# Kernel tuning notes

Hardware: AMD Instinct MI355X
Metric: run time of the kernel (lower is better)

## Reference

```python
import jax, jax.numpy as jnp
import numpy as np

# Note: the original applies F.dropout(p=0.2) after the shared Linear. Dropout is
# omitted here (identity) so the reference is deterministic; this is the eval-mode math.

def setup_inputs() -> dict:
    key = jax.random.key(0)
    k1, k2, k3 = jax.random.split(key, 3)
    B, L, D = 8, 2048, 1024  # D = dim*4 with dim=256
    ix = jax.random.normal(k1, (B, L, D), dtype=jnp.float32)
    iother = jax.random.normal(k2, (B, L, D), dtype=jnp.float32)
    # Linear(dim*4, dim*4) weight/bias, torch convention W: [out, in]
    W = jax.random.normal(k3, (D, D), dtype=jnp.float32) * (1.0 / np.sqrt(D))
    b = jnp.zeros((D,), dtype=jnp.float32)
    return {"ix": ix, "iother": iother, "W": W, "b": b}


def reference(ix, iother, W, b):
    # shared projection (torch Linear: x @ W.T + b)
    ex = ix @ W.T + b            # [B, Lx, D]
    eother = iother @ W.T + b    # [B, Lo, D]
    # cross-attention scores (no scaling, per original)
    align = jnp.einsum('bld,bmd->blm', ex, eother)   # [B, Lx, Lo]
    align = jax.nn.softmax(align, axis=-1)
    # note: values are the RAW iother, not the projected eother
    aligned = jnp.einsum('blm,bmd->bld', align, iother)  # [B, Lx, D]
    return aligned
```

## Files before the change

### kernel.cpp

```cpp
#include <hip/hip_runtime.h>
#include <stdint.h>
#include <stddef.h>


typedef short bf16x8 __attribute__((ext_vector_type(8)));
typedef float f32x4  __attribute__((ext_vector_type(4)));

typedef const __attribute__((address_space(1))) uint32_t* gas_ptr;
typedef __attribute__((address_space(3))) uint32_t* las_ptr;

__device__ __forceinline__ void gl_lds16(const void* g, void* l) {
    __builtin_amdgcn_global_load_lds((gas_ptr)g, (las_ptr)l, 16, 0, 0);
}

__device__ __forceinline__ unsigned short f2bf(float f) {
    union { float f; uint32_t u; } v; v.f = f;
    uint32_t r = v.u + 0x7fffu + ((v.u >> 16) & 1u);
    return (unsigned short)(r >> 16);
}
__device__ __forceinline__ float bf2f(unsigned short h) {
    union { uint32_t u; float f; } v; v.u = ((uint32_t)h) << 16; return v.f;
}

#define L_ 2048
#define D_ 1024
#define ROWB 4096
#define NKT 32
#define SLOT 49152
#define LDSB 32768
#define DYN_LDS (3 * SLOT)
#define SLOT2 65536
#define LDSB2 32768
#define DYN_LDS2 (2 * SLOT2)

__device__ __forceinline__ void xcd_remap(int gx, int gy, int& m, int& n, int& z) {
    const int bid = blockIdx.x + gx * (blockIdx.y + gy * blockIdx.z);
    const int T = gx * gy * (int)gridDim.z;
    const int chunk = T >> 3;
    const int b2 = (bid & 7) * chunk + (bid >> 3);
    m = b2 % gx;
    const int r = b2 / gx;
    n = r % gy;
    z = r / gy;
}

__global__ __launch_bounds__(256) void k_split(
        const float* __restrict__ in, unsigned short* __restrict__ hl, int n4) {
    const int i = blockIdx.x * 256 + threadIdx.x;
    if (i >= n4) return;
    float4 v = ((const float4*)in)[i];
    unsigned short h0 = f2bf(v.x), h1 = f2bf(v.y), h2 = f2bf(v.z), h3 = f2bf(v.w);
    unsigned short l0 = f2bf(v.x - bf2f(h0)), l1 = f2bf(v.y - bf2f(h1));
    unsigned short l2 = f2bf(v.z - bf2f(h2)), l3 = f2bf(v.w - bf2f(h3));
    uint2 hu, lu;
    hu.x = (uint32_t)h0 | ((uint32_t)h1 << 16);
    hu.y = (uint32_t)h2 | ((uint32_t)h3 << 16);
    lu.x = (uint32_t)l0 | ((uint32_t)l1 << 16);
    lu.y = (uint32_t)l2 | ((uint32_t)l3 << 16);
    const int row = i >> 8;
    const int c4 = (i & 255) << 2;
    const size_t o = (size_t)row * 2048 + ((c4 >> 5) << 6) + (c4 & 31);
    *(uint2*)&hl[o]      = hu;
    *(uint2*)&hl[o + 32] = lu;
}

__global__ __launch_bounds__(256) void k_transpose(
        const float* __restrict__ V, unsigned short* __restrict__ Vt) {
    __shared__ unsigned short tile[64][72];
    const int b = blockIdx.z, k0 = blockIdx.x * 64, n0 = blockIdx.y * 64;
    const int t = threadIdx.x;
    const int row = t >> 2, cs = (t & 3) * 16;
    const float* src = V + ((size_t)b * L_ + k0 + row) * D_ + n0 + cs;
#pragma unroll
    for (int q = 0; q < 4; q++) {
        float4 f = ((const float4*)src)[q];
        tile[row][cs + q * 4 + 0] = f2bf(f.x);
        tile[row][cs + q * 4 + 1] = f2bf(f.y);
        tile[row][cs + q * 4 + 2] = f2bf(f.z);
        tile[row][cs + q * 4 + 3] = f2bf(f.w);
    }
    __syncthreads();
    union { unsigned short us[16]; uint4 q[2]; } pk;
#pragma unroll
    for (int j = 0; j < 16; j++) pk.us[j] = tile[cs + j][row];
    unsigned short* dst = Vt + ((size_t)b * D_ + n0 + row) * L_ + k0 + cs;
    *(uint4*)dst       = pk.q[0];
    *(uint4*)(dst + 8) = pk.q[1];
}

__global__ __launch_bounds__(256) void k_tsplit(
        const float* __restrict__ W, unsigned short* __restrict__ Wt) {
    __shared__ float tile[64][68];
    const int n0 = blockIdx.x * 64, k0 = blockIdx.y * 64;
    const int t = threadIdx.x;
    const int row = t >> 2, cs = (t & 3) * 16;
    const float* src = W + ((size_t)(n0 + row)) * D_ + k0 + cs;
#pragma unroll
    for (int q = 0; q < 4; q++) {
        float4 f = ((const float4*)src)[q];
        tile[row][cs + q * 4 + 0] = f.x;
        tile[row][cs + q * 4 + 1] = f.y;
        tile[row][cs + q * 4 + 2] = f.z;
        tile[row][cs + q * 4 + 3] = f.w;
    }
    __syncthreads();
    union { unsigned short us[16]; uint4 q[2]; } hi, lo;
#pragma unroll
    for (int j = 0; j < 16; j++) {
        float v = tile[cs + j][row];
        unsigned short h = f2bf(v);
        hi.us[j] = h;
        lo.us[j] = f2bf(v - bf2f(h));
    }
    const int ng = n0 + cs;
    unsigned short* dst = Wt + (size_t)(k0 + row) * 2048 + ((ng >> 5) << 6) + (ng & 31);
    *(uint4*)dst        = hi.q[0];
    *(uint4*)(dst + 8)  = hi.q[1];
    *(uint4*)(dst + 32) = lo.q[0];
    *(uint4*)(dst + 40) = lo.q[1];
}

struct Frg { bf16x8 aH[4], aL[4], bH[4], bL[4]; };

template<int SP3>
__device__ __forceinline__ void mfma_cluster(const Frg& f, f32x4 (&acc)[4][4]) {
    __builtin_amdgcn_s_setprio(1);
#pragma unroll
    for (int i = 0; i < 4; i++)
#pragma unroll
        for (int j = 0; j < 4; j++) {
            f32x4 c = acc[i][j];
            if (SP3) {
                c = __builtin_amdgcn_mfma_f32_16x16x32_bf16(f.aH[i], f.bH[j], c, 0, 0, 0);
                c = __builtin_amdgcn_mfma_f32_16x16x32_bf16(f.aH[i], f.bL[j], c, 0, 0, 0);
                c = __builtin_amdgcn_mfma_f32_16x16x32_bf16(f.aL[i], f.bH[j], c, 0, 0, 0);
            } else {
                c = __builtin_amdgcn_mfma_f32_16x16x32_bf16(f.aH[i], f.bH[j], c, 0, 0, 0);
                c = __builtin_amdgcn_mfma_f32_16x16x32_bf16(f.aL[i], f.bL[j], c, 0, 0, 0);
            }
            acc[i][j] = c;
        }
    __builtin_amdgcn_s_setprio(0);
}

template<int SP3>
__device__ __forceinline__ void gemm_mainloop(
        const char* __restrict__ Ag, const char* __restrict__ Bg,
        f32x4 (&acc)[4][4], int kt0, int nkt) {
    extern __shared__ char smem[];
    const int t = threadIdx.x, lane = t & 63, w = t >> 6;
    const int l16 = lane & 15, quad = lane >> 4;
    const int mw = w >> 1, nw = w & 1;
    const int ln8 = lane >> 3, l8 = lane & 7;

    const int scol = (l8 * 16) ^ (ln8 << 4);
    const char* gA = Ag + (size_t)(w * 8 + ln8) * ROWB + scol;
    const char* gB = Bg + (size_t)(w * 8 + ln8) * ROWB + scol;
    const int sdst = w * 1024;

    const int swz  = (l16 & 7) << 4;
    const int colH = (quad * 16) ^ swz;
    const int colL = (64 + quad * 16) ^ swz;
    const int aRow = (mw * 64 + l16) * 128;
    const int bRow = LDSB + (nw * 64 + l16) * 128;

#pragma unroll
    for (int i = 0; i < 4; i++)
#pragma unroll
        for (int j = 0; j < 4; j++) acc[i][j] = (f32x4){0.f, 0.f, 0.f, 0.f};

    auto STAGE = [&](int soff, int ktAbs) {
        char* sb = smem + soff;
        const size_t gko = (size_t)ktAbs * 128;
#pragma unroll
        for (int q = 0; q < 4; q++)
            gl_lds16(gA + (size_t)q * (64 * ROWB) + gko, sb + q * 8192 + sdst);
#pragma unroll
        for (int q = 0; q < 2; q++)
            gl_lds16(gB + (size_t)q * (64 * ROWB) + gko, sb + LDSB + q * 8192 + sdst);
    };
    auto LDF = [&](int soff, Frg& f) {
        const char* cb = smem + soff;
#pragma unroll
        for (int i = 0; i < 4; i++) {
            const int ro = aRow + i * 2048;
            f.aH[i] = *(const bf16x8*)(cb + ro + colH);
            f.aL[i] = *(const bf16x8*)(cb + ro + colL);
        }
#pragma unroll
        for (int j = 0; j < 4; j++) {
            const int ro = bRow + j * 2048;
            f.bH[j] = *(const bf16x8*)(cb + ro + colH);
            f.bL[j] = *(const bf16x8*)(cb + ro + colL);
        }
    };

    STAGE(0, kt0 + 0);
    STAGE(SLOT, kt0 + 1);
    asm volatile("s_waitcnt vmcnt(6)" ::: "memory");
    __builtin_amdgcn_s_barrier();
    Frg fC, fN;
    LDF(0, fC);

    int ktr = 2 & (nkt - 1), sCur = 0;
#pragma unroll 1
    for (int it = 0; it < nkt / 2; ++it) {
        {
            int sStage = sCur + 2 * SLOT; if (sStage >= 3 * SLOT) sStage -= 3 * SLOT;
            int sLd    = sCur + SLOT;     if (sLd    >= 3 * SLOT) sLd    -= 3 * SLOT;
            STAGE(sStage, kt0 + ktr); ktr = (ktr + 1) & (nkt - 1);
            asm volatile("s_waitcnt vmcnt(6)" ::: "memory");
            asm volatile("s_waitcnt lgkmcnt(0)" ::: "memory");
            __builtin_amdgcn_s_barrier();
            LDF(sLd, fN);
            mfma_cluster<SP3>(fC, acc);
            sCur = sLd;
        }
        {
            int sStage = sCur + 2 * SLOT; if (sStage >= 3 * SLOT) sStage -= 3 * SLOT;
            int sLd    = sCur + SLOT;     if (sLd    >= 3 * SLOT) sLd    -= 3 * SLOT;
            STAGE(sStage, kt0 + ktr); ktr = (ktr + 1) & (nkt - 1);
            asm volatile("s_waitcnt vmcnt(6)" ::: "memory");
            asm volatile("s_waitcnt lgkmcnt(0)" ::: "memory");
            __builtin_amdgcn_s_barrier();
            LDF(sLd, fC);
            mfma_cluster<SP3>(fN, acc);
            sCur = sLd;
        }
    }
}

__device__ __forceinline__ void gemm_mainloop2(
        const char* __restrict__ Ag, const char* __restrict__ Bg,
        f32x4 (&acc)[8][4]) {
    extern __shared__ char smem[];
    const int t = threadIdx.x, lane = t & 63, w = t >> 6;
    const int l16 = lane & 15, quad = lane >> 4;
    const int mw = w >> 2, nw = w & 3;
    const int ln8 = lane >> 3, l8 = lane & 7;

    const int scol = (l8 * 16) ^ (ln8 << 4);
    const char* gA = Ag + (size_t)(w * 8 + ln8) * ROWB + scol;
    const char* gB = Bg + (size_t)(w * 8 + ln8) * ROWB + scol;
    const int sdst = w * 1024;

    const int swz  = (l16 & 7) << 4;
    const int colH = (quad * 16) ^ swz;
    const int colL = (64 + quad * 16) ^ swz;
    const int aRow = (mw * 128 + l16) * 128;
    const int bRow = LDSB2 + (nw * 64 + l16) * 128;

#pragma unroll
    for (int i = 0; i < 8; i++)
#pragma unroll
        for (int j = 0; j < 4; j++) acc[i][j] = (f32x4){0.f, 0.f, 0.f, 0.f};

    auto STAGE = [&](int soff, int ktAbs) {
        char* sb = smem + soff;
        const size_t gko = (size_t)ktAbs * 128;
#pragma unroll
        for (int q = 0; q < 4; q++)
            gl_lds16(gA + (size_t)q * (64 * ROWB) + gko, sb + q * 8192 + sdst);
#pragma unroll
        for (int q = 0; q < 4; q++)
            gl_lds16(gB + (size_t)q * (64 * ROWB) + gko, sb + LDSB2 + q * 8192 + sdst);
    };
    auto COMPUTE = [&](int soff) {
        const char* cb = smem + soff;
        bf16x8 bH[4], bL[4];
#pragma unroll
        for (int j = 0; j < 4; j++) {
            const int ro = bRow + j * 2048;
            bH[j] = *(const bf16x8*)(cb + ro + colH);
            bL[j] = *(const bf16x8*)(cb + ro + colL);
        }
#pragma unroll
        for (int h = 0; h < 2; h++) {
            bf16x8 aH[4], aL[4];
#pragma unroll
            for (int i = 0; i < 4; i++) {
                const int ro = aRow + h * 8192 + i * 2048;
                aH[i] = *(const bf16x8*)(cb + ro + colH);
                aL[i] = *(const bf16x8*)(cb + ro + colL);
            }
            __builtin_amdgcn_s_setprio(1);
#pragma unroll
            for (int i = 0; i < 4; i++)
#pragma unroll
                for (int j = 0; j < 4; j++) {
                    f32x4 c = acc[h * 4 + i][j];
                    c = __builtin_amdgcn_mfma_f32_16x16x32_bf16(aH[i], bH[j], c, 0, 0, 0);
                    c = __builtin_amdgcn_mfma_f32_16x16x32_bf16(aH[i], bL[j], c, 0, 0, 0);
                    c = __builtin_amdgcn_mfma_f32_16x16x32_bf16(aL[i], bH[j], c, 0, 0, 0);
                    acc[h * 4 + i][j] = c;
                }
            __builtin_amdgcn_s_setprio(0);
        }
    };

    STAGE(0, 0);
    int ktn = 1;
#pragma unroll 1
    for (int it = 0; it < NKT / 2; ++it) {
        STAGE(SLOT2, ktn); ktn = (ktn + 1) & (NKT - 1);
        asm volatile("s_waitcnt vmcnt(8)" ::: "memory");
        __builtin_amdgcn_s_barrier();
        COMPUTE(0);
        asm volatile("s_waitcnt lgkmcnt(0)" ::: "memory");
        __builtin_amdgcn_s_barrier();
        STAGE(0, ktn); ktn = (ktn + 1) & (NKT - 1);
        asm volatile("s_waitcnt vmcnt(8)" ::: "memory");
        __builtin_amdgcn_s_barrier();
        COMPUTE(SLOT2);
        asm volatile("s_waitcnt lgkmcnt(0)" ::: "memory");
        __builtin_amdgcn_s_barrier();
    }
}

__global__ __launch_bounds__(512, 2) void k_wtw(
        const char* __restrict__ Wt, float* __restrict__ Mpart, int nkt) {
    const int M0 = blockIdx.x * 256, N0 = blockIdx.y * 128, z = blockIdx.z;
    f32x4 acc[4][4];
    gemm_mainloop<1>(Wt + (size_t)M0 * ROWB, Wt + (size_t)N0 * ROWB, acc, z * nkt, nkt);

    const int t = threadIdx.x, lane = t & 63, w = t >> 6;
    const int l16 = lane & 15, quad = lane >> 4, mw = w >> 1, nw = w & 1;
    float* Sp = Mpart + ((size_t)z << 20)
              + (size_t)(M0 + mw * 64 + quad * 4) * 1024 + N0 + nw * 64;
#pragma unroll
    for (int i = 0; i < 4; i++)
#pragma unroll
        for (int j = 0; j < 4; j++)
#pragma unroll
            for (int r = 0; r < 4; r++)
                Sp[(size_t)(i * 16 + r) * 1024 + j * 16 + l16] = acc[i][j][r];
}

__global__ __launch_bounds__(256) void k_mreduce(
        const float* __restrict__ Mpart, unsigned short* __restrict__ Mhl, int zn) {
    const int i = blockIdx.x;
    const int j = threadIdx.x * 4;
    float4 s = {0.f, 0.f, 0.f, 0.f};
    for (int z = 0; z < zn; z++) {
        float4 v = *(const float4*)(Mpart + ((size_t)z << 20) + (size_t)i * 1024 + j);
        s.x += v.x; s.y += v.y; s.z += v.z; s.w += v.w;
    }
    unsigned short h0 = f2bf(s.x), h1 = f2bf(s.y), h2 = f2bf(s.z), h3 = f2bf(s.w);
    unsigned short l0 = f2bf(s.x - bf2f(h0)), l1 = f2bf(s.y - bf2f(h1));
    unsigned short l2 = f2bf(s.z - bf2f(h2)), l3 = f2bf(s.w - bf2f(h3));
    uint2 hu, lu;
    hu.x = (uint32_t)h0 | ((uint32_t)h1 << 16);
    hu.y = (uint32_t)h2 | ((uint32_t)h3 << 16);
    lu.x = (uint32_t)l0 | ((uint32_t)l1 << 16);
    lu.y = (uint32_t)l2 | ((uint32_t)l3 << 16);
    const size_t o = (size_t)i * 2048 + ((j >> 5) << 6) + (j & 31);
    *(uint2*)&Mhl[o]      = hu;
    *(uint2*)&Mhl[o + 32] = lu;
}

__global__ __launch_bounds__(256) void k_wtb(
        const float* __restrict__ W, const float* __restrict__ b,
        float* __restrict__ c) {
    const int k = blockIdx.x * 256 + threadIdx.x;
    const int n0 = blockIdx.y * 128;
    float s = 0.f;
#pragma unroll 4
    for (int n = 0; n < 128; n++) s += b[n0 + n] * W[(size_t)(n0 + n) * D_ + k];
    atomicAdd(&c[k], s);
}

__global__ __launch_bounds__(256) void k_v2(
        const float* __restrict__ io, const float* __restrict__ c,
        float* __restrict__ v2) {
    __shared__ float cs[1024];
    const int t = threadIdx.x;
#pragma unroll
    for (int q = 0; q < 4; q++) cs[q * 256 + t] = c[q * 256 + t];
    __syncthreads();
    const int r = blockIdx.x * 4 + (t >> 6);
    const int lane = t & 63;
    const float* row = io + (size_t)r * D_ + lane * 16;
    float s = 0.f;
#pragma unroll
    for (int q = 0; q < 4; q++) {
        float4 v = ((const float4*)row)[q];
        s += v.x * cs[lane * 16 + q * 4 + 0] + v.y * cs[lane * 16 + q * 4 + 1]
           + v.z * cs[lane * 16 + q * 4 + 2] + v.w * cs[lane * 16 + q * 4 + 3];
    }
#pragma unroll
    for (int o = 32; o > 0; o >>= 1) s += __shfl_xor(s, o, 64);
    if (lane == 0) v2[r] = s;
}

__global__ __launch_bounds__(512, 2) void k_gproj(
        const char* __restrict__ Ahl, const char* __restrict__ Mhl,
        unsigned short* __restrict__ Ehl) {
    const int M0 = blockIdx.x * 256, N0 = blockIdx.y * 128;
    f32x4 acc[4][4];
    gemm_mainloop<1>(Ahl + (size_t)M0 * ROWB, Mhl + (size_t)N0 * ROWB, acc, 0, NKT);

    const int t = threadIdx.x, lane = t & 63, w = t >> 6;
    const int l16 = lane & 15, quad = lane >> 4, mw = w >> 1, nw = w & 1;
#pragma unroll
    for (int j = 0; j < 4; j++) {
        const int n = N0 + nw * 64 + j * 16 + l16;
        unsigned short* eb = Ehl + (size_t)(M0 + mw * 64 + quad * 4) * 2048
                             + (size_t)(n >> 5) * 64 + (n & 31);
#pragma unroll
        for (int i = 0; i < 4; i++)
#pragma unroll
            for (int r = 0; r < 4; r++) {
                float v = acc[i][j][r];
                unsigned short h  = f2bf(v);
                unsigned short lo = f2bf(v - bf2f(h));
                unsigned short* p = eb + (size_t)(i * 16 + r) * 2048;
                p[0]  = h;
                p[32] = lo;
            }
    }
}

__global__ __launch_bounds__(512, 2) void k_gscores(
        const char* __restrict__ Ehl, const char* __restrict__ Ohl,
        const float* __restrict__ v2, float* __restrict__ S) {
    int mb, nb_, zb;
    xcd_remap(L_ / 256, L_ / 256, mb, nb_, zb);
    const int M0 = mb * 256, N0 = nb_ * 256, bb = zb;
    const char* Ae = Ehl + (size_t)(bb * L_ + M0) * ROWB;
    const char* Be = Ohl + (size_t)(bb * L_ + N0) * ROWB;
    f32x4 acc[8][4];
    gemm_mainloop2(Ae, Be, acc);

    const int t = threadIdx.x, lane = t & 63, w = t >> 6;
    const int l16 = lane & 15, quad = lane >> 4, mw = w >> 2, nw = w & 3;
    float* Sp = S + ((size_t)bb * L_ + M0 + mw * 128 + quad * 4) * (size_t)L_
                  + N0 + nw * 64;
    const float* v2p = v2 + (size_t)bb * L_ + N0 + nw * 64;
#pragma unroll
    for (int j = 0; j < 4; j++) {
        const float vb = v2p[j * 16 + l16];
#pragma unroll
        for (int i = 0; i < 8; i++)
#pragma unroll
            for (int r = 0; r < 4; r++)
                Sp[(size_t)(i * 16 + r) * L_ + j * 16 + l16] = acc[i][j][r] + vb;
    }
}

__global__ __launch_bounds__(256) void k_rowsoftmax(
        const float* __restrict__ S, unsigned short* __restrict__ P) {
    const size_t r = blockIdx.x;
    const float* row = S + r * (size_t)L_;
    const int t = threadIdx.x, lane = t & 63, wave = t >> 6;
    float4 v0 = ((const float4*)row)[t];
    float4 v1 = ((const float4*)row)[t + 256];
    float mx = fmaxf(fmaxf(fmaxf(v0.x, v0.y), fmaxf(v0.z, v0.w)),
                     fmaxf(fmaxf(v1.x, v1.y), fmaxf(v1.z, v1.w)));
#pragma unroll
    for (int o = 32; o > 0; o >>= 1) mx = fmaxf(mx, __shfl_xor(mx, o, 64));
    __shared__ float red[4];
    __shared__ float bmax, binv;
    if (lane == 0) red[wave] = mx;
    __syncthreads();
    if (t == 0) bmax = fmaxf(fmaxf(red[0], red[1]), fmaxf(red[2], red[3]));
    __syncthreads();
    const float m = bmax;
    float e0x = __expf(fminf(v0.x - m, 0.f)), e0y = __expf(fminf(v0.y - m, 0.f));
    float e0z = __expf(fminf(v0.z - m, 0.f)), e0w = __expf(fminf(v0.w - m, 0.f));
    float e1x = __expf(fminf(v1.x - m, 0.f)), e1y = __expf(fminf(v1.y - m, 0.f));
    float e1z = __expf(fminf(v1.z - m, 0.f)), e1w = __expf(fminf(v1.w - m, 0.f));
    float s = e0x + e0y + e0z + e0w + e1x + e1y + e1z + e1w;
#pragma unroll
    for (int o = 32; o > 0; o >>= 1) s += __shfl_xor(s, o, 64);
    __syncthreads();
    if (lane == 0) red[wave] = s;
    __syncthreads();
    if (t == 0) binv = 1.0f / (red[0] + red[1] + red[2] + red[3]);
    __syncthreads();
    const float ril = binv;
    uint2 a, b;
    a.x = (uint32_t)f2bf(e0x * ril) | ((uint32_t)f2bf(e0y * ril) << 16);
    a.y = (uint32_t)f2bf(e0z * ril) | ((uint32_t)f2bf(e0w * ril) << 16);
    b.x = (uint32_t)f2bf(e1x * ril) | ((uint32_t)f2bf(e1y * ril) << 16);
    b.y = (uint32_t)f2bf(e1z * ril) | ((uint32_t)f2bf(e1w * ril) << 16);
    uint2* pr = (uint2*)(P + r * (size_t)L_);
    pr[t]       = a;
    pr[t + 256] = b;
}

__global__ __launch_bounds__(512, 2) void k_pvg(
        const char* __restrict__ Pbf, const char* __restrict__ Vt,
        float* __restrict__ out) {
    int mb, nb_, zb;
    xcd_remap(L_ / 256, D_ / 128, mb, nb_, zb);
    const int M0 = mb * 256, N0 = nb_ * 128, bb = zb;
    const char* Ae = Pbf + ((size_t)bb * L_ + M0) * ROWB;
    const char* Be = Vt + ((size_t)bb * D_ + N0) * ROWB;
    f32x4 acc[4][4];
    gemm_mainloop<0>(Ae, Be, acc, 0, NKT);

    const int t = threadIdx.x, lane = t & 63, w = t >> 6;
    const int l16 = lane & 15, quad = lane >> 4, mw = w >> 1, nw = w & 1;
    float* op = out + ((size_t)bb * L_ + M0 + mw * 64 + quad * 4) * (size_t)D_
                    + N0 + nw * 64;
#pragma unroll
    for (int i = 0; i < 4; i++)
#pragma unroll
        for (int j = 0; j < 4; j++)
#pragma unroll
            for (int r = 0; r < 4; r++)
                op[(size_t)(i * 16 + r) * D_ + j * 16 + l16] = acc[i][j][r];
}

extern "C" void kernel_launch(void* const* d_in, const int* in_sizes, int n_in,
                              void* d_out, int out_size, void* d_ws, size_t ws_size,
                              hipStream_t stream) {
    const float* ix   = (const float*)d_in[0];
    const float* io   = (const float*)d_in[1];
    const float* W    = (const float*)d_in[2];
    const float* bias = (const float*)d_in[3];
    float* out = (float*)d_out;

    hipFuncSetAttribute((const void*)k_gproj,
                        hipFuncAttributeMaxDynamicSharedMemorySize, DYN_LDS);
    hipFuncSetAttribute((const void*)k_gscores,
                        hipFuncAttributeMaxDynamicSharedMemorySize, DYN_LDS2);
    hipFuncSetAttribute((const void*)k_wtw,
                        hipFuncAttributeMaxDynamicSharedMemorySize, DYN_LDS);
    hipFuncSetAttribute((const void*)k_pvg,
                        hipFuncAttributeMaxDynamicSharedMemorySize, DYN_LDS);

    const size_t MB = 1024 * 1024;
    const size_t PB_EI = (size_t)L_ * ROWB;
    const size_t PB_S  = (size_t)L_ * L_ * 4;
    const size_t PB_E  = (size_t)L_ * D_ * 2;
    const size_t PB_ST = (size_t)L_ * 4;

    int nb = 8;
    while (nb > 1) {
        size_t need = 4 * MB + (size_t)nb * (2 * PB_EI + PB_S + PB_E + 2 * PB_ST) + 8192;
        if (need <= ws_size) break;
        nb >>= 1;
    }

    char* ws = (char*)d_ws;
    size_t off = 0;
    unsigned short* Mhl = (unsigned short*)(ws + off); off += 4 * MB;
    unsigned short* EHL = (unsigned short*)(ws + off); off += (size_t)nb * PB_EI;
    unsigned short* OHL = (unsigned short*)(ws + off); off += (size_t)nb * PB_EI;
    char* regA = ws + off;                             off += (size_t)nb * PB_S;
    unsigned short* Vt = (unsigned short*)(ws + off);  off += (size_t)nb * PB_E;
    float* v2   = (float*)(ws + off);                  off += (size_t)nb * PB_ST;
    float* cvec = (float*)(ws + off);                  off += 4096;
    unsigned short* WtHL = EHL;
    float* Mpart = (float*)OHL;
    unsigned short* Pbf = EHL;
    const int zsplit = (nb >= 2) ? 8 : 4;
    const int nktc = NKT / zsplit;

    k_tsplit<<<dim3(16, 16), 256, 0, stream>>>(W, WtHL);
    k_wtw<<<dim3(4, 8, zsplit), 512, DYN_LDS, stream>>>((const char*)WtHL, Mpart, nktc);
    k_mreduce<<<1024, 256, 0, stream>>>(Mpart, Mhl, zsplit);
    hipMemsetAsync(cvec, 0, D_ * sizeof(float), stream);
    k_wtb<<<dim3(4, 8), 256, 0, stream>>>(W, bias, cvec);

    for (int b0 = 0; b0 < 8; b0 += nb) {
        const float* ixc = ix + (size_t)b0 * L_ * D_;
        const float* ioc = io + (size_t)b0 * L_ * D_;
        float* outc = out + (size_t)b0 * L_ * D_;
        const int nLD4 = nb * L_ * D_ / 4;
        const int nbL = nb * L_;
        float* S = (float*)regA;

        k_split<<<nb * 2048, 256, 0, stream>>>(ixc, (unsigned short*)regA, nLD4);
        k_split<<<nb * 2048, 256, 0, stream>>>(ioc, OHL, nLD4);
        k_transpose<<<dim3(32, 16, nb), 256, 0, stream>>>(ioc, Vt);
        k_v2<<<nbL / 4, 256, 0, stream>>>(ioc, cvec, v2);
        k_gproj<<<dim3(nbL / 256, D_ / 128), 512, DYN_LDS, stream>>>(
            (const char*)regA, (const char*)Mhl, EHL);
        k_gscores<<<dim3(L_ / 256, L_ / 256, nb), 512, DYN_LDS2, stream>>>(
            (const char*)EHL, (const char*)OHL, v2, S);
        k_rowsoftmax<<<2048 * nb, 256, 0, stream>>>(S, Pbf);
        k_pvg<<<dim3(L_ / 256, D_ / 128, nb), 512, DYN_LDS, stream>>>(
            (const char*)Pbf, (const char*)Vt, outc);
    }
}
```

Measured before the change: 605.2 us.

## Move projection and PV GEMMs to 256x256 tiles and widen split kernel

The projection GEMM and the P·V GEMM now use the larger 256x256-tile mainloop already used by the scores GEMM, with an SP3 template flag selecting 3-term or 2-term split-bf16 MFMA sequences. Larger tiles raise data reuse per LDS stage and cut the number of blocks, at the cost of more accumulator registers and the loss of the XCD remap in k_pvg. The fp32-to-hi/lo split kernel now handles 8 elements per thread with 16-byte stores, which reduces the thread count and store instructions.

```diff
diff --git a/kernel.cpp b/kernel.cpp
--- a/kernel.cpp
+++ b/kernel.cpp
@@ -45,23 +45,32 @@
 }
 
 __global__ __launch_bounds__(256) void k_split(
-        const float* __restrict__ in, unsigned short* __restrict__ hl, int n4) {
+        const float* __restrict__ in, unsigned short* __restrict__ hl, int n8) {
     const int i = blockIdx.x * 256 + threadIdx.x;
-    if (i >= n4) return;
-    float4 v = ((const float4*)in)[i];
-    unsigned short h0 = f2bf(v.x), h1 = f2bf(v.y), h2 = f2bf(v.z), h3 = f2bf(v.w);
-    unsigned short l0 = f2bf(v.x - bf2f(h0)), l1 = f2bf(v.y - bf2f(h1));
-    unsigned short l2 = f2bf(v.z - bf2f(h2)), l3 = f2bf(v.w - bf2f(h3));
-    uint2 hu, lu;
-    hu.x = (uint32_t)h0 | ((uint32_t)h1 << 16);
-    hu.y = (uint32_t)h2 | ((uint32_t)h3 << 16);
-    lu.x = (uint32_t)l0 | ((uint32_t)l1 << 16);
-    lu.y = (uint32_t)l2 | ((uint32_t)l3 << 16);
-    const int row = i >> 8;
-    const int c4 = (i & 255) << 2;
-    const size_t o = (size_t)row * 2048 + ((c4 >> 5) << 6) + (c4 & 31);
-    *(uint2*)&hl[o]      = hu;
-    *(uint2*)&hl[o + 32] = lu;
+    if (i >= n8) return;
+    const float4* p = (const float4*)in + (size_t)i * 2;
+    float4 va = p[0], vb = p[1];
+    unsigned short h[8], l[8];
+    const float f[8] = {va.x, va.y, va.z, va.w, vb.x, vb.y, vb.z, vb.w};
+#pragma unroll
+    for (int q = 0; q < 8; q++) {
+        h[q] = f2bf(f[q]);
+        l[q] = f2bf(f[q] - bf2f(h[q]));
+    }
+    uint4 hu, lu;
+    hu.x = (uint32_t)h[0] | ((uint32_t)h[1] << 16);
+    hu.y = (uint32_t)h[2] | ((uint32_t)h[3] << 16);
+    hu.z = (uint32_t)h[4] | ((uint32_t)h[5] << 16);
+    hu.w = (uint32_t)h[6] | ((uint32_t)h[7] << 16);
+    lu.x = (uint32_t)l[0] | ((uint32_t)l[1] << 16);
+    lu.y = (uint32_t)l[2] | ((uint32_t)l[3] << 16);
+    lu.z = (uint32_t)l[4] | ((uint32_t)l[5] << 16);
+    lu.w = (uint32_t)l[6] | ((uint32_t)l[7] << 16);
+    const int row = i >> 7;
+    const int c = (i & 127) << 3;
+    const size_t o = (size_t)row * 2048 + ((c >> 5) << 6) + (c & 31);
+    *(uint4*)&hl[o]      = hu;
+    *(uint4*)&hl[o + 32] = lu;
 }
 
 __global__ __launch_bounds__(256) void k_transpose(
@@ -122,28 +131,21 @@
 
 struct Frg { bf16x8 aH[4], aL[4], bH[4], bL[4]; };
 
-template<int SP3>
-__device__ __forceinline__ void mfma_cluster(const Frg& f, f32x4 (&acc)[4][4]) {
+__device__ __forceinline__ void mfma48(const Frg& f, f32x4 (&acc)[4][4]) {
     __builtin_amdgcn_s_setprio(1);
 #pragma unroll
     for (int i = 0; i < 4; i++)
 #pragma unroll
         for (int j = 0; j < 4; j++) {
             f32x4 c = acc[i][j];
-            if (SP3) {
-                c = __builtin_amdgcn_mfma_f32_16x16x32_bf16(f.aH[i], f.bH[j], c, 0, 0, 0);
-                c = __builtin_amdgcn_mfma_f32_16x16x32_bf16(f.aH[i], f.bL[j], c, 0, 0, 0);
-                c = __builtin_amdgcn_mfma_f32_16x16x32_bf16(f.aL[i], f.bH[j], c, 0, 0, 0);
-            } else {
-                c = __builtin_amdgcn_mfma_f32_16x16x32_bf16(f.aH[i], f.bH[j], c, 0, 0, 0);
-                c = __builtin_amdgcn_mfma_f32_16x16x32_bf16(f.aL[i], f.bL[j], c, 0, 0, 0);
-            }
+            c = __builtin_amdgcn_mfma_f32_16x16x32_bf16(f.aH[i], f.bH[j], c, 0, 0, 0);
+            c = __builtin_amdgcn_mfma_f32_16x16x32_bf16(f.aH[i], f.bL[j], c, 0, 0, 0);
+            c = __builtin_amdgcn_mfma_f32_16x16x32_bf16(f.aL[i], f.bH[j], c, 0, 0, 0);
             acc[i][j] = c;
         }
     __builtin_amdgcn_s_setprio(0);
 }
 
-template<int SP3>
 __device__ __forceinline__ void gemm_mainloop(
         const char* __restrict__ Ag, const char* __restrict__ Bg,
         f32x4 (&acc)[4][4], int kt0, int nkt) {
@@ -213,7 +215,7 @@
             asm volatile("s_waitcnt lgkmcnt(0)" ::: "memory");
             __builtin_amdgcn_s_barrier();
             LDF(sLd, fN);
-            mfma_cluster<SP3>(fC, acc);
+            mfma48(fC, acc);
             sCur = sLd;
         }
         {
@@ -224,12 +226,13 @@
             asm volatile("s_waitcnt lgkmcnt(0)" ::: "memory");
             __builtin_amdgcn_s_barrier();
             LDF(sLd, fC);
-            mfma_cluster<SP3>(fN, acc);
+            mfma48(fN, acc);
             sCur = sLd;
         }
     }
 }
 
+template<int SP3>
 __device__ __forceinline__ void gemm_mainloop2(
         const char* __restrict__ Ag, const char* __restrict__ Bg,
         f32x4 (&acc)[8][4]) {
@@ -289,9 +292,14 @@
 #pragma unroll
                 for (int j = 0; j < 4; j++) {
                     f32x4 c = acc[h * 4 + i][j];
-                    c = __builtin_amdgcn_mfma_f32_16x16x32_bf16(aH[i], bH[j], c, 0, 0, 0);
-                    c = __builtin_amdgcn_mfma_f32_16x16x32_bf16(aH[i], bL[j], c, 0, 0, 0);
-                    c = __builtin_amdgcn_mfma_f32_16x16x32_bf16(aL[i], bH[j], c, 0, 0, 0);
+                    if (SP3) {
+                        c = __builtin_amdgcn_mfma_f32_16x16x32_bf16(aH[i], bH[j], c, 0, 0, 0);
+                        c = __builtin_amdgcn_mfma_f32_16x16x32_bf16(aH[i], bL[j], c, 0, 0, 0);
+                        c = __builtin_amdgcn_mfma_f32_16x16x32_bf16(aL[i], bH[j], c, 0, 0, 0);
+                    } else {
+                        c = __builtin_amdgcn_mfma_f32_16x16x32_bf16(aH[i], bH[j], c, 0, 0, 0);
+                        c = __builtin_amdgcn_mfma_f32_16x16x32_bf16(aL[i], bL[j], c, 0, 0, 0);
+                    }
                     acc[h * 4 + i][j] = c;
                 }
             __builtin_amdgcn_s_setprio(0);
@@ -321,7 +329,7 @@
         const char* __restrict__ Wt, float* __restrict__ Mpart, int nkt) {
     const int M0 = blockIdx.x * 256, N0 = blockIdx.y * 128, z = blockIdx.z;
     f32x4 acc[4][4];
-    gemm_mainloop<1>(Wt + (size_t)M0 * ROWB, Wt + (size_t)N0 * ROWB, acc, z * nkt, nkt);
+    gemm_mainloop(Wt + (size_t)M0 * ROWB, Wt + (size_t)N0 * ROWB, acc, z * nkt, nkt);
 
     const int t = threadIdx.x, lane = t & 63, w = t >> 6;
     const int l16 = lane & 15, quad = lane >> 4, mw = w >> 1, nw = w & 1;
@@ -395,19 +403,19 @@
 __global__ __launch_bounds__(512, 2) void k_gproj(
         const char* __restrict__ Ahl, const char* __restrict__ Mhl,
         unsigned short* __restrict__ Ehl) {
-    const int M0 = blockIdx.x * 256, N0 = blockIdx.y * 128;
-    f32x4 acc[4][4];
-    gemm_mainloop<1>(Ahl + (size_t)M0 * ROWB, Mhl + (size_t)N0 * ROWB, acc, 0, NKT);
+    const int M0 = blockIdx.x * 256, N0 = blockIdx.y * 256;
+    f32x4 acc[8][4];
+    gemm_mainloop2<1>(Ahl + (size_t)M0 * ROWB, Mhl + (size_t)N0 * ROWB, acc);
 
     const int t = threadIdx.x, lane = t & 63, w = t >> 6;
-    const int l16 = lane & 15, quad = lane >> 4, mw = w >> 1, nw = w & 1;
+    const int l16 = lane & 15, quad = lane >> 4, mw = w >> 2, nw = w & 3;
 #pragma unroll
     for (int j = 0; j < 4; j++) {
         const int n = N0 + nw * 64 + j * 16 + l16;
-        unsigned short* eb = Ehl + (size_t)(M0 + mw * 64 + quad * 4) * 2048
+        unsigned short* eb = Ehl + (size_t)(M0 + mw * 128 + quad * 4) * 2048
                              + (size_t)(n >> 5) * 64 + (n & 31);
 #pragma unroll
-        for (int i = 0; i < 4; i++)
+        for (int i = 0; i < 8; i++)
 #pragma unroll
             for (int r = 0; r < 4; r++) {
                 float v = acc[i][j][r];
@@ -429,7 +437,7 @@
     const char* Ae = Ehl + (size_t)(bb * L_ + M0) * ROWB;
     const char* Be = Ohl + (size_t)(bb * L_ + N0) * ROWB;
     f32x4 acc[8][4];
-    gemm_mainloop2(Ae, Be, acc);
+    gemm_mainloop2<1>(Ae, Be, acc);
 
     const int t = threadIdx.x, lane = t & 63, w = t >> 6;
     const int l16 = lane & 15, quad = lane >> 4, mw = w >> 2, nw = w & 3;
@@ -491,20 +499,18 @@
 __global__ __launch_bounds__(512, 2) void k_pvg(
         const char* __restrict__ Pbf, const char* __restrict__ Vt,
         float* __restrict__ out) {
-    int mb, nb_, zb;
-    xcd_remap(L_ / 256, D_ / 128, mb, nb_, zb);
-    const int M0 = mb * 256, N0 = nb_ * 128, bb = zb;
+    const int M0 = blockIdx.x * 256, N0 = blockIdx.y * 256, bb = blockIdx.z;
     const char* Ae = Pbf + ((size_t)bb * L_ + M0) * ROWB;
     const char* Be = Vt + ((size_t)bb * D_ + N0) * ROWB;
-    f32x4 acc[4][4];
-    gemm_mainloop<0>(Ae, Be, acc, 0, NKT);
+    f32x4 acc[8][4];
+    gemm_mainloop2<0>(Ae, Be, acc);
 
     const int t = threadIdx.x, lane = t & 63, w = t >> 6;
-    const int l16 = lane & 15, quad = lane >> 4, mw = w >> 1, nw = w & 1;
-    float* op = out + ((size_t)bb * L_ + M0 + mw * 64 + quad * 4) * (size_t)D_
+    const int l16 = lane & 15, quad = lane >> 4, mw = w >> 2, nw = w & 3;
+    float* op = out + ((size_t)bb * L_ + M0 + mw * 128 + quad * 4) * (size_t)D_
                     + N0 + nw * 64;
 #pragma unroll
-    for (int i = 0; i < 4; i++)
+    for (int i = 0; i < 8; i++)
 #pragma unroll
         for (int j = 0; j < 4; j++)
 #pragma unroll
@@ -522,13 +528,13 @@
     float* out = (float*)d_out;
 
     hipFuncSetAttribute((const void*)k_gproj,
-                        hipFuncAttributeMaxDynamicSharedMemorySize, DYN_LDS);
+                        hipFuncAttributeMaxDynamicSharedMemorySize, DYN_LDS2);
     hipFuncSetAttribute((const void*)k_gscores,
                         hipFuncAttributeMaxDynamicSharedMemorySize, DYN_LDS2);
     hipFuncSetAttribute((const void*)k_wtw,
                         hipFuncAttributeMaxDynamicSharedMemorySize, DYN_LDS);
     hipFuncSetAttribute((const void*)k_pvg,
-                        hipFuncAttributeMaxDynamicSharedMemorySize, DYN_LDS);
+                        hipFuncAttributeMaxDynamicSharedMemorySize, DYN_LDS2);
 
     const size_t MB = 1024 * 1024;
     const size_t PB_EI = (size_t)L_ * ROWB;
@@ -568,20 +574,20 @@
         const float* ixc = ix + (size_t)b0 * L_ * D_;
         const float* ioc = io + (size_t)b0 * L_ * D_;
         float* outc = out + (size_t)b0 * L_ * D_;
-        const int nLD4 = nb * L_ * D_ / 4;
+        const int nLD8 = nb * L_ * D_ / 8;
         const int nbL = nb * L_;
         float* S = (float*)regA;
 
-        k_split<<<nb * 2048, 256, 0, stream>>>(ixc, (unsigned short*)regA, nLD4);
-        k_split<<<nb * 2048, 256, 0, stream>>>(ioc, OHL, nLD4);
+        k_split<<<nLD8 / 256, 256, 0, stream>>>(ixc, (unsigned short*)regA, nLD8);
+        k_split<<<nLD8 / 256, 256, 0, stream>>>(ioc, OHL, nLD8);
         k_transpose<<<dim3(32, 16, nb), 256, 0, stream>>>(ioc, Vt);
         k_v2<<<nbL / 4, 256, 0, stream>>>(ioc, cvec, v2);
-        k_gproj<<<dim3(nbL / 256, D_ / 128), 512, DYN_LDS, stream>>>(
+        k_gproj<<<dim3(nbL / 256, D_ / 256), 512, DYN_LDS2, stream>>>(
             (const char*)regA, (const char*)Mhl, EHL);
         k_gscores<<<dim3(L_ / 256, L_ / 256, nb), 512, DYN_LDS2, stream>>>(
             (const char*)EHL, (const char*)OHL, v2, S);
         k_rowsoftmax<<<2048 * nb, 256, 0, stream>>>(S, Pbf);
-        k_pvg<<<dim3(L_ / 256, D_ / 128, nb), 512, DYN_LDS, stream>>>(
+        k_pvg<<<dim3(L_ / 256, D_ / 256, nb), 512, DYN_LDS2, stream>>>(
             (const char*)Pbf, (const char*)Vt, outc);
     }
 }
```

New measurement: 702.5 us. 1.16x slower.
